# Optimization experiments

Measured on AMD Instinct MI355X. Metric: run time of the kernel, lower is better.

Reference implementation:

```python
import jax, jax.numpy as jnp
import numpy as np
from jax import lax

N = 8192
D_IN, H1, H2 = 512, 256, 128
NSTEPS = 5  # args.n; module holds NSTEPS+1 weight pairs


def setup_inputs() -> dict:
    key = jax.random.key(0)
    k1, k2, k3, k4, k5, k6 = jax.random.split(key, 6)
    X = jax.random.normal(k1, (N, D_IN), dtype=jnp.float32)
    # dense normalized adjacency surrogate: row sums ~1 to keep activations sane
    adj = jax.random.uniform(k2, (N, N), dtype=jnp.float32) * (2.0 / N)
    # glorot-ish scaled weights, stacked per timestep (indices 0..NSTEPS)
    W1 = jax.random.normal(k3, (NSTEPS + 1, D_IN, H1), dtype=jnp.float32) * np.float32(np.sqrt(2.0 / (D_IN + H1)))
    W2 = jax.random.normal(k4, (NSTEPS + 1, H1, H2), dtype=jnp.float32) * np.float32(np.sqrt(2.0 / (H1 + H2)))
    cum_sqrt = jax.random.uniform(k5, (NSTEPS + 1,), dtype=jnp.float32) + 0.5
    sqrt_omac = jax.random.uniform(k6, (NSTEPS + 1,), dtype=jnp.float32)
    return {"X": X, "adj": adj, "W1": W1, "W2": W2,
            "cum_sqrt": cum_sqrt, "sqrt_omac": sqrt_omac,
            "time_step": 1, "timesteps": NSTEPS}


def reference(X, adj, W1, W2, cum_sqrt, sqrt_omac, time_step, timesteps):
    # get_value_at_index(tensor, i) == tensor[i-1]
    denom = cum_sqrt[time_step - 1]
    # static slices (time_step/timesteps are Python ints)
    Ws1 = W1[time_step:timesteps + 1]            # [T, D_IN, H1]
    Ws2 = W2[time_step:timesteps + 1]            # [T, H1, H2]
    coefs = sqrt_omac[time_step - 1:timesteps]   # [T]

    def step(acc, wc):
        w1, w2, c = wc
        h1 = jax.nn.relu(adj @ (X @ w1))         # [N, H1]
        h2 = jax.nn.relu(adj @ (h1 @ w2))        # [N, H2]
        a = h2 - h2.mean(axis=0, keepdims=True)  # center per feature
        acc = acc + c * jax.nn.sigmoid(a @ a.T)  # [N, N]
        return acc, None

    acc0 = jnp.zeros((X.shape[0], X.shape[0]), dtype=X.dtype)
    predicted_adj, _ = lax.scan(step, acc0, (Ws1, Ws2, coefs))
    return predicted_adj / denom
```

## Files before the change

### kernel.cpp

```cpp
#include <hip/hip_runtime.h>

typedef short v8s __attribute__((ext_vector_type(8)));
typedef float v4f __attribute__((ext_vector_type(4)));
typedef int   v4i __attribute__((ext_vector_type(4)));
typedef int   v8i __attribute__((ext_vector_type(8)));
typedef unsigned short u16;
typedef unsigned char  u8;

#define BM 128
#define BN 128
#define BK 64
#define LP 132

#define SCALE_M13 0x72727272
#define SCALE_0   0x7F7F7F7F
#define SCALE_M6  0x79797979
#define SCALE_M12 0x73737373

__device__ __forceinline__ u16 f2bf(float f) {
  union { float f; unsigned int u; } v; v.f = f;
  unsigned int r = (v.u + 0x7FFFu + ((v.u >> 16) & 1u)) >> 16;
  return (u16)r;
}
__device__ __forceinline__ float bf2f(u16 b) {
  union { unsigned int u; float f; } v; v.u = ((unsigned int)b) << 16;
  return v.f;
}
__device__ __forceinline__ unsigned int pk4fp8(float a, float b, float c, float d) {
  unsigned int p = __builtin_amdgcn_cvt_pk_fp8_f32(a, b, 0, false);
  p = __builtin_amdgcn_cvt_pk_fp8_f32(c, d, p, true);
  return p;
}

__device__ __forceinline__ void gld16(const void* g, void* l) {
  __builtin_amdgcn_global_load_lds(
      (const __attribute__((address_space(1))) void*)g,
      (__attribute__((address_space(3))) void*)l, 16, 0, 0);
}

__device__ __forceinline__ v8i ldfrag8(const u8* S, int m, int q) {
  const int s0 = (2 * q) ^ (m & 7);
  const v4i lo = *(const v4i*)(S + m * 128 + s0 * 16);
  const v4i hi = *(const v4i*)(S + m * 128 + (s0 ^ 1) * 16);
  v8i r;
  r[0] = lo[0]; r[1] = lo[1]; r[2] = lo[2]; r[3] = lo[3];
  r[4] = hi[0]; r[5] = hi[1]; r[6] = hi[2]; r[7] = hi[3];
  return r;
}


__global__ void cvt_f32_bf16_x8(const float* __restrict__ in, u16* __restrict__ out, long n8) {
  const long i = (long)blockIdx.x * 256 + threadIdx.x;
  if (i >= n8) return;
  const float4 x = ((const float4*)in)[i * 2];
  const float4 y = ((const float4*)in)[i * 2 + 1];
  v8s o;
  o[0] = (short)f2bf(x.x); o[1] = (short)f2bf(x.y);
  o[2] = (short)f2bf(x.z); o[3] = (short)f2bf(x.w);
  o[4] = (short)f2bf(y.x); o[5] = (short)f2bf(y.y);
  o[6] = (short)f2bf(y.z); o[7] = (short)f2bf(y.w);
  ((v8s*)out)[i] = o;
}

__global__ void cvt_f32_fp8_x8(const float* __restrict__ in, u8* __restrict__ out,
                               float scale, long n8) {
  const long i = (long)blockIdx.x * 256 + threadIdx.x;
  if (i >= n8) return;
  const float4 x = ((const float4*)in)[i * 2];
  const float4 y = ((const float4*)in)[i * 2 + 1];
  uint2 p;
  p.x = pk4fp8(x.x * scale, x.y * scale, x.z * scale, x.w * scale);
  p.y = pk4fp8(y.x * scale, y.y * scale, y.z * scale, y.w * scale);
  ((uint2*)out)[i] = p;
}

__global__ void packW1(const float* __restrict__ W1, u16* __restrict__ W1t) {
  const int idx = blockIdx.x * 256 + threadIdx.x;
  const int k = idx & 511, sn = idx >> 9;
  const int s = sn >> 8, n = sn & 255;
  W1t[idx] = f2bf(W1[((long)(1 + s) * 512 + k) * 256 + n]);
}

__global__ void packW2(const float* __restrict__ W2, u16* __restrict__ W2t) {
  const int idx = blockIdx.x * 256 + threadIdx.x;
  const int k = idx & 255, sn = idx >> 8;
  const int s = sn >> 7, n = sn & 127;
  W2t[idx] = f2bf(W2[((long)(1 + s) * 256 + k) * 128 + n]);
}


__global__ __launch_bounds__(256, 3) void gemm_bt_o8(
    const u16* __restrict__ A, long lda, long zA,
    const u16* __restrict__ B, long ldb, long zB,
    u8* __restrict__ C, long ldc, long zC, int K, float oscale) {
  __shared__ u16 As[BM * BK];
  __shared__ u16 Bs[BN * BK];
  const int tid = threadIdx.x;
  const long m0 = (long)blockIdx.y * BM;
  const long n0 = (long)blockIdx.x * BN;
  const u16* Ap = A + (long)blockIdx.z * zA;
  const u16* Bp = B + (long)blockIdx.z * zB;

  const int wave = tid >> 6, lane = tid & 63;
  const int wr = wave >> 1, wc = wave & 1;
  const int lq = lane >> 4, lr = lane & 15;

  v4f acc[4][4] = {};

  for (int k0 = 0; k0 < K; k0 += BK) {
    __syncthreads();
#pragma unroll
    for (int i = 0; i < 4; ++i) {
      const int c = i * 256 + tid;
      const int row = c >> 3, j = c & 7;
      const int kc = j ^ (row & 7);
      gld16(Ap + (m0 + row) * lda + (k0 + kc * 8), &As[c * 8]);
      gld16(Bp + (n0 + row) * ldb + (k0 + kc * 8), &Bs[c * 8]);
    }
    __syncthreads();
#pragma unroll
    for (int kk = 0; kk < 2; ++kk) {
      v8s a[4], b[4];
#pragma unroll
      for (int mi = 0; mi < 4; ++mi) {
        const int m = wr * 64 + mi * 16 + lr;
        const int ch = m * 8 + ((kk * 4 + lq) ^ (m & 7));
        a[mi] = *(const v8s*)&As[ch * 8];
      }
#pragma unroll
      for (int ni = 0; ni < 4; ++ni) {
        const int n = wc * 64 + ni * 16 + lr;
        const int ch = n * 8 + ((kk * 4 + lq) ^ (n & 7));
        b[ni] = *(const v8s*)&Bs[ch * 8];
      }
#pragma unroll
      for (int mi = 0; mi < 4; ++mi)
#pragma unroll
        for (int ni = 0; ni < 4; ++ni)
          acc[mi][ni] = __builtin_amdgcn_mfma_f32_16x16x32_bf16(a[mi], b[ni], acc[mi][ni], 0, 0, 0);
    }
  }

  u8* Cp = C + (long)blockIdx.z * zC;
#pragma unroll
  for (int ni = 0; ni < 4; ++ni) {
    const long n = n0 + wc * 64 + ni * 16 + lr;
#pragma unroll
    for (int mi = 0; mi < 4; ++mi) {
      const long mb = m0 + wr * 64 + mi * 16 + lq * 4;
      const unsigned int p = pk4fp8(acc[mi][ni][0] * oscale, acc[mi][ni][1] * oscale,
                                    acc[mi][ni][2] * oscale, acc[mi][ni][3] * oscale);
      *(unsigned int*)&Cp[n * ldc + mb] = p;
    }
  }
}


__global__ __launch_bounds__(256, 3) void gemm_fp8(
    const u8* __restrict__ A, long lda,
    const u8* __restrict__ B, long ldb,
    u16* __restrict__ C, long ldc, int K, int sa, int sb) {
  __shared__ u8 As[128 * 128];
  __shared__ u8 Bs[128 * 128];
  const int tid = threadIdx.x;
  const long m0 = (long)blockIdx.y * 128;
  const long n0 = (long)blockIdx.x * 128;
  const int wave = tid >> 6, lane = tid & 63;
  const int wr = wave >> 1, wc = wave & 1;
  const int lq = lane >> 4, lr = lane & 15;

  v4f acc[4][4] = {};

  for (int k0 = 0; k0 < K; k0 += 128) {
    __syncthreads();
#pragma unroll
    for (int i = 0; i < 4; ++i) {
      const int c = i * 256 + tid;
      const int row = c >> 3, j = c & 7;
      const int kc = j ^ (row & 7);
      gld16(A + (m0 + row) * lda + (k0 + kc * 16), &As[c * 16]);
      gld16(B + (n0 + row) * ldb + (k0 + kc * 16), &Bs[c * 16]);
    }
    __syncthreads();
    v8i a[4];
#pragma unroll
    for (int mi = 0; mi < 4; ++mi)
      a[mi] = ldfrag8(As, wr * 64 + mi * 16 + lr, lq);
#pragma unroll
    for (int ni = 0; ni < 4; ++ni) {
      const v8i b = ldfrag8(Bs, wc * 64 + ni * 16 + lr, lq);
#pragma unroll
      for (int mi = 0; mi < 4; ++mi)
        acc[mi][ni] = __builtin_amdgcn_mfma_scale_f32_16x16x128_f8f6f4(
            a[mi], b, acc[mi][ni], 0, 0, 0, sa, 0, sb);
    }
  }

#pragma unroll
  for (int mi = 0; mi < 4; ++mi) {
    const long mb = m0 + wr * 64 + mi * 16 + lq * 4;
#pragma unroll
    for (int ni = 0; ni < 4; ++ni) {
      const long n = n0 + wc * 64 + ni * 16 + lr;
#pragma unroll
      for (int r = 0; r < 4; ++r) {
        float v = acc[mi][ni][r];
        v = v > 0.f ? v : 0.f;
        C[(mb + r) * ldc + n] = f2bf(v);
      }
    }
  }
}


__global__ void colsum(const u16* __restrict__ H, float* __restrict__ sums) {
  const int c = blockIdx.x * 64 + (threadIdx.x & 63);
  const int rt = threadIdx.x >> 6;
  const int r0 = blockIdx.y * 256;
  float s = 0.f;
  for (int r = r0 + rt; r < r0 + 256; r += 4) s += bf2f(H[(long)r * 640 + c]);
  __shared__ float red[256];
  red[threadIdx.x] = s;
  __syncthreads();
  if (threadIdx.x < 64) {
    float t = red[threadIdx.x] + red[threadIdx.x + 64] + red[threadIdx.x + 128] + red[threadIdx.x + 192];
    atomicAdd(&sums[c], t);
  }
}

__global__ void subme(const u16* __restrict__ H, const float* __restrict__ sums,
                      u8* __restrict__ O) {
  const long i4 = ((long)blockIdx.x * 256 + threadIdx.x) * 4;
  const int c = (int)(i4 % 640);
  const float inv = 1.0f / 8192.0f;
  const float a0 = (bf2f(H[i4 + 0]) - sums[c + 0] * inv) * 4096.0f;
  const float a1 = (bf2f(H[i4 + 1]) - sums[c + 1] * inv) * 4096.0f;
  const float a2 = (bf2f(H[i4 + 2]) - sums[c + 2] * inv) * 4096.0f;
  const float a3 = (bf2f(H[i4 + 3]) - sums[c + 3] * inv) * 4096.0f;
  *(unsigned int*)&O[i4] = pk4fp8(a0, a1, a2, a3);
}


__global__ __launch_bounds__(256, 2) void g5_fp8(
    const u8* __restrict__ A8,
    const float* __restrict__ som,
    const float* __restrict__ cum,
    float* __restrict__ out) {
  const int bx = blockIdx.x, by = blockIdx.y;
  if (by > bx) return;

  __shared__ __align__(16) char smem[34048];
  u8* As = (u8*)smem;
  u8* Bs = As + 16384;
  float* Lf = (float*)smem;

  const int tid = threadIdx.x;
  const long m0 = (long)by * BM;
  const long n0 = (long)bx * BN;
  const int wave = tid >> 6, lane = tid & 63;
  const int wr = wave >> 1, wc = wave & 1;
  const int lq = lane >> 4, lr = lane & 15;
  const float invden = 1.0f / cum[0];
  const float NL2E = -1.4426950408889634f;

  v4f oacc[4][4] = {};
  for (int s = 0; s < 5; ++s) {
    const float cs = som[s];
    __syncthreads();
#pragma unroll
    for (int i = 0; i < 4; ++i) {
      const int c = i * 256 + tid;
      const int row = c >> 3, j = c & 7;
      const int kc = j ^ (row & 7);
      gld16(A8 + (m0 + row) * 640 + (s * 128 + kc * 16), &As[c * 16]);
      gld16(A8 + (n0 + row) * 640 + (s * 128 + kc * 16), &Bs[c * 16]);
    }
    __syncthreads();
    v8i a[4];
#pragma unroll
    for (int mi = 0; mi < 4; ++mi)
      a[mi] = ldfrag8(As, wr * 64 + mi * 16 + lr, lq);
    v4f acc[4][4] = {};
#pragma unroll
    for (int ni = 0; ni < 4; ++ni) {
      const v8i b = ldfrag8(Bs, wc * 64 + ni * 16 + lr, lq);
#pragma unroll
      for (int mi = 0; mi < 4; ++mi)
        acc[mi][ni] = __builtin_amdgcn_mfma_scale_f32_16x16x128_f8f6f4(
            a[mi], b, acc[mi][ni], 0, 0, 0, SCALE_M12, 0, SCALE_M12);
    }
#pragma unroll
    for (int mi = 0; mi < 4; ++mi)
#pragma unroll
      for (int ni = 0; ni < 4; ++ni)
#pragma unroll
        for (int r = 0; r < 4; ++r) {
          const float z = acc[mi][ni][r];
          const float e = __builtin_amdgcn_exp2f(z * NL2E);
          oacc[mi][ni][r] += cs * __builtin_amdgcn_rcpf(1.0f + e);
        }
  }

  const bool mirror = (bx > by);
#pragma unroll
  for (int h = 0; h < 2; ++h) {
    __syncthreads();
    if (wr == h) {
#pragma unroll
      for (int mi = 0; mi < 4; ++mi)
#pragma unroll
        for (int ni = 0; ni < 4; ++ni) {
          const int lcol = wc * 64 + ni * 16 + lr;
#pragma unroll
          for (int r = 0; r < 4; ++r) {
            const int lrow = mi * 16 + lq * 4 + r;
            Lf[lrow * LP + lcol] = oacc[mi][ni][r] * invden;
          }
        }
    }
    __syncthreads();
    {
      const int row = tid >> 2;
      const int cb = (tid & 3) * 32;
      float* op = out + (m0 + h * 64 + row) * 8192L + n0 + cb;
      const float* lp = &Lf[row * LP + cb];
#pragma unroll
      for (int i = 0; i < 8; ++i)
        ((float4*)op)[i] = *(const float4*)(lp + i * 4);
    }
    if (mirror) {
#pragma unroll
      for (int p = 0; p < 2; ++p) {
        const int c = p * 64 + (tid >> 2);
        const int rb = (tid & 3) * 16;
        float t0[16];
#pragma unroll
        for (int j = 0; j < 16; ++j) t0[j] = Lf[(rb + j) * LP + c];
        float* op = out + (n0 + c) * 8192L + m0 + h * 64 + rb;
        ((float4*)op)[0] = make_float4(t0[0], t0[1], t0[2], t0[3]);
        ((float4*)op)[1] = make_float4(t0[4], t0[5], t0[6], t0[7]);
        ((float4*)op)[2] = make_float4(t0[8], t0[9], t0[10], t0[11]);
        ((float4*)op)[3] = make_float4(t0[12], t0[13], t0[14], t0[15]);
      }
    }
  }
}


extern "C" void kernel_launch(void* const* d_in, const int* in_sizes, int n_in,
                              void* d_out, int out_size, void* d_ws, size_t ws_size,
                              hipStream_t stream) {
  const float* X   = (const float*)d_in[0];
  const float* adj = (const float*)d_in[1];
  const float* W1  = (const float*)d_in[2];
  const float* W2  = (const float*)d_in[3];
  const float* cum = (const float*)d_in[4];
  const float* som = (const float*)d_in[5];

  char* ob = (char*)d_out;
  u8*  adjb8 = (u8*)(ob);
  u8*  T1t8  = (u8*)(ob + 67108864);
  u16* H1    = (u16*)(ob + 77594624);
  u8*  T2t8  = (u8*)(ob + 98566144);
  u16* Xb    = (u16*)(ob + 103809024);
  u16* Acat  = (u16*)(ob + 112197632);

  char* wb = (char*)d_ws;
  u16* W1t   = (u16*)(wb);
  u16* W2t   = (u16*)(wb + 1310720);
  u8*  Acat8 = (u8*)(wb + 1638400);
  float* sums = (float*)(wb + 6881280);

  cvt_f32_fp8_x8<<<32768, 256, 0, stream>>>(adj, adjb8, 8192.0f, 8388608);
  cvt_f32_bf16_x8<<<2048, 256, 0, stream>>>(X, Xb, 524288);
  packW1<<<2560, 256, 0, stream>>>(W1, W1t);
  packW2<<<640, 256, 0, stream>>>(W2, W2t);

  gemm_bt_o8<<<dim3(10, 64, 1), 256, 0, stream>>>(Xb, 512, 0, W1t, 512, 0,
                                                  T1t8, 8192, 0, 512, 1.0f);
  gemm_fp8<<<dim3(10, 64), 256, 0, stream>>>(adjb8, 8192, T1t8, 8192,
                                             H1, 1280, 8192, SCALE_M13, SCALE_0);
  gemm_bt_o8<<<dim3(1, 64, 5), 256, 0, stream>>>(H1, 1280, 256, W2t, 256, 128 * 256,
                                                 T2t8, 8192, (long)128 * 8192, 256, 64.0f);
  gemm_fp8<<<dim3(5, 64), 256, 0, stream>>>(adjb8, 8192, T2t8, 8192,
                                            Acat, 640, 8192, SCALE_M13, SCALE_M6);

  hipMemsetAsync(sums, 0, 640 * sizeof(float), stream);
  colsum<<<dim3(10, 32), 256, 0, stream>>>(Acat, sums);
  subme<<<5120, 256, 0, stream>>>(Acat, sums, Acat8);

  g5_fp8<<<dim3(64, 64), 256, 0, stream>>>(Acat8, som, cum, (float*)d_out);
}
```

Baseline: 821.7 us.

## Drop LDS staging in final sigmoid GEMM and launch only upper-triangle tiles

The final kernel now loads its MFMA fragments straight from global memory instead of staging them through LDS with barriers. It launches only the 2080 upper-triangle blocks and recovers (by, bx) with a sqrt-based index formula, so no blocks exit early. The epilogue writes accumulators directly to global memory, with float4 stores for the mirrored transpose, rather than going through an LDS transpose buffer. This removes shared-memory traffic and synchronisation, at the cost of less coalesced direct stores, especially the scalar-strided ones for the non-mirrored half.

```diff
diff --git a/kernel.cpp b/kernel.cpp
--- a/kernel.cpp
+++ b/kernel.cpp
@@ -1,4 +1,5 @@
 #include <hip/hip_runtime.h>
+#include <math.h>
 
 typedef short v8s __attribute__((ext_vector_type(8)));
 typedef float v4f __attribute__((ext_vector_type(4)));
@@ -10,7 +11,6 @@
 #define BM 128
 #define BN 128
 #define BK 64
-#define LP 132
 
 #define SCALE_M13 0x72727272
 #define SCALE_0   0x7F7F7F7F
@@ -42,6 +42,15 @@
   const int s0 = (2 * q) ^ (m & 7);
   const v4i lo = *(const v4i*)(S + m * 128 + s0 * 16);
   const v4i hi = *(const v4i*)(S + m * 128 + (s0 ^ 1) * 16);
+  v8i r;
+  r[0] = lo[0]; r[1] = lo[1]; r[2] = lo[2]; r[3] = lo[3];
+  r[4] = hi[0]; r[5] = hi[1]; r[6] = hi[2]; r[7] = hi[3];
+  return r;
+}
+
+__device__ __forceinline__ v8i ldfrag_g(const u8* __restrict__ p) {
+  const v4i lo = *(const v4i*)p;
+  const v4i hi = *(const v4i*)(p + 16);
   v8i r;
   r[0] = lo[0]; r[1] = lo[1]; r[2] = lo[2]; r[3] = lo[3];
   r[4] = hi[0]; r[5] = hi[1]; r[6] = hi[2]; r[7] = hi[3];
@@ -246,13 +255,11 @@
     const float* __restrict__ som,
     const float* __restrict__ cum,
     float* __restrict__ out) {
-  const int bx = blockIdx.x, by = blockIdx.y;
-  if (by > bx) return;
-
-  __shared__ __align__(16) char smem[34048];
-  u8* As = (u8*)smem;
-  u8* Bs = As + 16384;
-  float* Lf = (float*)smem;
+  const int bid = blockIdx.x;
+  int by = (int)(64.5f - sqrtf(64.5f * 64.5f - 2.0f * (float)bid));
+  while ((by + 1) * (129 - (by + 1)) / 2 <= bid) ++by;
+  while (by * (129 - by) / 2 > bid) --by;
+  const int bx = by + (bid - by * (129 - by) / 2);
 
   const int tid = threadIdx.x;
   const long m0 = (long)by * BM;
@@ -263,32 +270,33 @@
   const float invden = 1.0f / cum[0];
   const float NL2E = -1.4426950408889634f;
 
+  const u8* arow[4];
+  const u8* brow[4];
+#pragma unroll
+  for (int mi = 0; mi < 4; ++mi)
+    arow[mi] = A8 + (m0 + wr * 64 + mi * 16 + lr) * 640 + lq * 32;
+#pragma unroll
+  for (int ni = 0; ni < 4; ++ni)
+    brow[ni] = A8 + (n0 + wc * 64 + ni * 16 + lr) * 640 + lq * 32;
+
   v4f oacc[4][4] = {};
+#pragma unroll
   for (int s = 0; s < 5; ++s) {
     const float cs = som[s];
-    __syncthreads();
-#pragma unroll
-    for (int i = 0; i < 4; ++i) {
-      const int c = i * 256 + tid;
-      const int row = c >> 3, j = c & 7;
-      const int kc = j ^ (row & 7);
-      gld16(A8 + (m0 + row) * 640 + (s * 128 + kc * 16), &As[c * 16]);
-      gld16(A8 + (n0 + row) * 640 + (s * 128 + kc * 16), &Bs[c * 16]);
-    }
-    __syncthreads();
-    v8i a[4];
-#pragma unroll
-    for (int mi = 0; mi < 4; ++mi)
-      a[mi] = ldfrag8(As, wr * 64 + mi * 16 + lr, lq);
+    v8i a[4], b[4];
+#pragma unroll
+    for (int mi = 0; mi < 4; ++mi) a[mi] = ldfrag_g(arow[mi] + s * 128);
+#pragma unroll
+    for (int ni = 0; ni < 4; ++ni) b[ni] = ldfrag_g(brow[ni] + s * 128);
+
     v4f acc[4][4] = {};
 #pragma unroll
-    for (int ni = 0; ni < 4; ++ni) {
-      const v8i b = ldfrag8(Bs, wc * 64 + ni * 16 + lr, lq);
+    for (int ni = 0; ni < 4; ++ni)
 #pragma unroll
       for (int mi = 0; mi < 4; ++mi)
         acc[mi][ni] = __builtin_amdgcn_mfma_scale_f32_16x16x128_f8f6f4(
-            a[mi], b, acc[mi][ni], 0, 0, 0, SCALE_M12, 0, SCALE_M12);
-    }
+            a[mi], b[ni], acc[mi][ni], 0, 0, 0, SCALE_M12, 0, SCALE_M12);
+
 #pragma unroll
     for (int mi = 0; mi < 4; ++mi)
 #pragma unroll
@@ -301,46 +309,30 @@
         }
   }
 
-  const bool mirror = (bx > by);
-#pragma unroll
-  for (int h = 0; h < 2; ++h) {
-    __syncthreads();
-    if (wr == h) {
-#pragma unroll
-      for (int mi = 0; mi < 4; ++mi)
-#pragma unroll
-        for (int ni = 0; ni < 4; ++ni) {
-          const int lcol = wc * 64 + ni * 16 + lr;
-#pragma unroll
-          for (int r = 0; r < 4; ++r) {
-            const int lrow = mi * 16 + lq * 4 + r;
-            Lf[lrow * LP + lcol] = oacc[mi][ni][r] * invden;
-          }
-        }
-    }
-    __syncthreads();
-    {
-      const int row = tid >> 2;
-      const int cb = (tid & 3) * 32;
-      float* op = out + (m0 + h * 64 + row) * 8192L + n0 + cb;
-      const float* lp = &Lf[row * LP + cb];
-#pragma unroll
-      for (int i = 0; i < 8; ++i)
-        ((float4*)op)[i] = *(const float4*)(lp + i * 4);
-    }
-    if (mirror) {
-#pragma unroll
-      for (int p = 0; p < 2; ++p) {
-        const int c = p * 64 + (tid >> 2);
-        const int rb = (tid & 3) * 16;
-        float t0[16];
-#pragma unroll
-        for (int j = 0; j < 16; ++j) t0[j] = Lf[(rb + j) * LP + c];
-        float* op = out + (n0 + c) * 8192L + m0 + h * 64 + rb;
-        ((float4*)op)[0] = make_float4(t0[0], t0[1], t0[2], t0[3]);
-        ((float4*)op)[1] = make_float4(t0[4], t0[5], t0[6], t0[7]);
-        ((float4*)op)[2] = make_float4(t0[8], t0[9], t0[10], t0[11]);
-        ((float4*)op)[3] = make_float4(t0[12], t0[13], t0[14], t0[15]);
+#pragma unroll
+  for (int mi = 0; mi < 4; ++mi) {
+    const long mb = m0 + wr * 64 + mi * 16 + lq * 4;
+#pragma unroll
+    for (int r = 0; r < 4; ++r)
+#pragma unroll
+      for (int ni = 0; ni < 4; ++ni) {
+        const long n = n0 + wc * 64 + ni * 16 + lr;
+        out[(mb + r) * 8192 + n] = oacc[mi][ni][r] * invden;
+      }
+  }
+  if (bx > by) {
+#pragma unroll
+    for (int ni = 0; ni < 4; ++ni) {
+      const long n = n0 + wc * 64 + ni * 16 + lr;
+#pragma unroll
+      for (int mi = 0; mi < 4; ++mi) {
+        const long mb = m0 + wr * 64 + mi * 16 + lq * 4;
+        float4 v;
+        v.x = oacc[mi][ni][0] * invden;
+        v.y = oacc[mi][ni][1] * invden;
+        v.z = oacc[mi][ni][2] * invden;
+        v.w = oacc[mi][ni][3] * invden;
+        *(float4*)&out[n * 8192 + mb] = v;
       }
     }
   }
@@ -389,5 +381,5 @@
   colsum<<<dim3(10, 32), 256, 0, stream>>>(Acat, sums);
   subme<<<5120, 256, 0, stream>>>(Acat, sums, Acat8);
 
-  g5_fp8<<<dim3(64, 64), 256, 0, stream>>>(Acat8, som, cum, (float*)d_out);
-}
+  g5_fp8<<<2080, 256, 0, stream>>>(Acat8, som, cum, (float*)d_out);
+}
```

Result: slower. 904.7 us (+10.1%).
